# Performance work log

Measured on AMD Instinct MI355X. Metric: run time of the kernel, lower is better.

The kernel has to match this reference:

```python
import jax, jax.numpy as jnp
import numpy as np

EPS = 1e-12  # match torch BCE's protection against log(0)


def setup_inputs() -> dict:
    key = jax.random.key(0)
    k1, k2 = jax.random.split(key)
    n = 8192
    # Pstar is the BCE `input` (prediction) -> must be in (0,1)
    Pstar = jax.random.uniform(k1, (n, n), dtype=jnp.float32)
    pred_pos = jax.random.uniform(k2, (n, 3), dtype=jnp.float32)
    return {"Pstar": Pstar, "pred_pos": pred_pos}


def compute_low_dim_adj(y):
    # Student-t / Cauchy affinity kernel: Q_ij = 1 / (1 + ||y_i - y_j||^2)
    sq = jnp.sum(y * y, axis=1)                      # [n]
    d2 = sq[:, None] + sq[None, :] - 2.0 * (y @ y.T)  # [n, n]
    d2 = jnp.maximum(d2, 0.0)
    return 1.0 / (1.0 + d2)


def reference(Pstar, pred_pos):
    Q = compute_low_dim_adj(pred_pos)  # target in (0,1]
    # F.binary_cross_entropy(input=Pstar, target=Q, reduction='mean')
    P = jnp.clip(Pstar, EPS, 1.0 - EPS)
    ce = -jnp.mean(Q * jnp.log(P) + (1.0 - Q) * jnp.log1p(-P))
    return ce, pred_pos
```

## Files before the change

kernel.cpp:

```cpp
#include <hip/hip_runtime.h>

constexpr int NN   = 8192;
constexpr int ROWS = 16;
constexpr int COLS = 1024;
constexpr int NBLK = (NN / ROWS) * (NN / COLS);
constexpr int COPYBLKS = (NN * 3) / 256;


__global__ __launch_bounds__(256, 8)
void bce_tsne_kernel(const float* __restrict__ Pstar,
                     const float* __restrict__ pos,
                     float* __restrict__ out)
{
    __shared__ float4 rowC[ROWS];
    __shared__ float  waveSum[4];

    const int tid = threadIdx.x;
    const int bid = blockIdx.x;
    const int rowBase = (bid >> 3) * ROWS;
    const int colBase = (bid & 7) * COLS;

    if (tid < ROWS) {
        const int i = rowBase + tid;
        const float y0 = pos[i * 3 + 0];
        const float y1 = pos[i * 3 + 1];
        const float y2 = pos[i * 3 + 2];
        rowC[tid] = make_float4(fmaf(y0, y0, fmaf(y1, y1, y2 * y2)),
                                -2.0f * y0, -2.0f * y1, -2.0f * y2);
    }

    const int j0 = colBase + tid * 4;
    const float4 f0 = *(const float4*)(pos + (size_t)j0 * 3);
    const float4 f1 = *(const float4*)(pos + (size_t)j0 * 3 + 4);
    const float4 f2 = *(const float4*)(pos + (size_t)j0 * 3 + 8);
    float ya[4] = {f0.x, f0.w, f1.z, f2.y};
    float yb[4] = {f0.y, f1.x, f1.w, f2.z};
    float yc[4] = {f0.z, f1.y, f2.x, f2.w};
    float sq[4];
    #pragma unroll
    for (int e = 0; e < 4; ++e)
        sq[e] = fmaf(ya[e], ya[e], fmaf(yb[e], yb[e], yc[e] * yc[e]));

    __syncthreads();

    float acc[4] = {0.0f, 0.0f, 0.0f, 0.0f};
    const float* prow = Pstar + (size_t)rowBase * NN + j0;

    #pragma unroll 4
    for (int r = 0; r < ROWS; ++r) {
        const float4 c  = rowC[r];
        const float4 p4 = *(const float4*)(prow + (size_t)r * NN);
        const float pp[4] = {p4.x, p4.y, p4.z, p4.w};
        #pragma unroll
        for (int e = 0; e < 4; ++e) {
            float d2 = c.x + sq[e];
            d2 = fmaf(c.y, ya[e], d2);
            d2 = fmaf(c.z, yb[e], d2);
            d2 = fmaf(c.w, yc[e], d2);
            d2 = fmaxf(d2, 0.0f);
            const float q  = __builtin_amdgcn_rcpf(1.0f + d2);
            const float p  = fmaxf(pp[e], 1e-12f);
            const float lp = __log2f(p);
            const float lm = __log2f(1.0f - p);
            acc[e] = fmaf(q, lp - lm, acc[e] + lm);
        }
    }

    float a = (acc[0] + acc[1]) + (acc[2] + acc[3]);
    #pragma unroll
    for (int off = 32; off > 0; off >>= 1)
        a += __shfl_down(a, off);
    const int lane = tid & 63;
    const int wid  = tid >> 6;
    if (lane == 0) waveSum[wid] = a;
    __syncthreads();
    if (tid == 0) {
        const float bp = waveSum[0] + waveSum[1] + waveSum[2] + waveSum[3];
        atomicAdd(out, bp * (-0.69314718055994531f / 67108864.0f));
    }

    if (bid < COPYBLKS) {
        const int k = bid * 256 + tid;
        out[1 + k] = pos[k];
    }
}

extern "C" void kernel_launch(void* const* d_in, const int* in_sizes, int n_in,
                              void* d_out, int out_size, void* d_ws, size_t ws_size,
                              hipStream_t stream) {
    const float* Pstar = (const float*)d_in[0];
    const float* pos   = (const float*)d_in[1];
    float* out = (float*)d_out;

    hipMemsetAsync(out, 0, sizeof(float), stream);
    bce_tsne_kernel<<<NBLK, 256, 0, stream>>>(Pstar, pos, out);
}
```

Before: 362.3 us.

## Double-buffer Pstar row loads, double rows per block, fold +1 into row constant

Each block now handles 32 rows instead of 16, which halves the grid and the number of atomics. Rows are processed in groups of four, and the next group's float4 loads are issued before the current group is computed, so memory latency is explicitly software-pipelined. The +1 of the Cauchy kernel is folded into the per-row constant, with the clamp changed to max(w, 1), which saves one add per element. Launch bounds are relaxed from 8 to 4 waves per EU to make room for the extra registers the buffers need, so occupancy may drop.

```diff
diff --git a/kernel.cpp b/kernel.cpp
--- a/kernel.cpp
+++ b/kernel.cpp
@@ -1,13 +1,35 @@
 #include <hip/hip_runtime.h>
 
 constexpr int NN   = 8192;
-constexpr int ROWS = 16;
+constexpr int ROWS = 32;
 constexpr int COLS = 1024;
 constexpr int NBLK = (NN / ROWS) * (NN / COLS);
 constexpr int COPYBLKS = (NN * 3) / 256;
+constexpr int GROUPS = ROWS / 4;
 
 
-__global__ __launch_bounds__(256, 8)
+__device__ __forceinline__ void bce4(const float4 p4, const float4 c,
+                                     const float ya[4], const float yb[4],
+                                     const float yc[4], const float sq[4],
+                                     float acc[4])
+{
+    const float pp[4] = {p4.x, p4.y, p4.z, p4.w};
+    #pragma unroll
+    for (int e = 0; e < 4; ++e) {
+        float w = c.x + sq[e];
+        w = fmaf(c.y, ya[e], w);
+        w = fmaf(c.z, yb[e], w);
+        w = fmaf(c.w, yc[e], w);
+        w = fmaxf(w, 1.0f);
+        const float q  = __builtin_amdgcn_rcpf(w);
+        const float p  = fmaxf(pp[e], 1e-12f);
+        const float lp = __log2f(p);
+        const float lm = __log2f(1.0f - p);
+        acc[e] = fmaf(q, lp - lm, acc[e] + lm);
+    }
+}
+
+__global__ __launch_bounds__(256, 4)
 void bce_tsne_kernel(const float* __restrict__ Pstar,
                      const float* __restrict__ pos,
                      float* __restrict__ out)
@@ -25,7 +47,7 @@
         const float y0 = pos[i * 3 + 0];
         const float y1 = pos[i * 3 + 1];
         const float y2 = pos[i * 3 + 2];
-        rowC[tid] = make_float4(fmaf(y0, y0, fmaf(y1, y1, y2 * y2)),
+        rowC[tid] = make_float4(fmaf(y0, y0, fmaf(y1, y1, fmaf(y2, y2, 1.0f))),
                                 -2.0f * y0, -2.0f * y1, -2.0f * y2);
     }
 
@@ -46,25 +68,26 @@
     float acc[4] = {0.0f, 0.0f, 0.0f, 0.0f};
     const float* prow = Pstar + (size_t)rowBase * NN + j0;
 
-    #pragma unroll 4
-    for (int r = 0; r < ROWS; ++r) {
-        const float4 c  = rowC[r];
-        const float4 p4 = *(const float4*)(prow + (size_t)r * NN);
-        const float pp[4] = {p4.x, p4.y, p4.z, p4.w};
+    float4 bufA[4];
+    #pragma unroll
+    for (int k = 0; k < 4; ++k)
+        bufA[k] = *(const float4*)(prow + (size_t)k * NN);
+
+    for (int g = 0; g < GROUPS - 1; ++g) {
+        float4 bufB[4];
+        const float* pn = prow + (size_t)(g + 1) * 4 * NN;
         #pragma unroll
-        for (int e = 0; e < 4; ++e) {
-            float d2 = c.x + sq[e];
-            d2 = fmaf(c.y, ya[e], d2);
-            d2 = fmaf(c.z, yb[e], d2);
-            d2 = fmaf(c.w, yc[e], d2);
-            d2 = fmaxf(d2, 0.0f);
-            const float q  = __builtin_amdgcn_rcpf(1.0f + d2);
-            const float p  = fmaxf(pp[e], 1e-12f);
-            const float lp = __log2f(p);
-            const float lm = __log2f(1.0f - p);
-            acc[e] = fmaf(q, lp - lm, acc[e] + lm);
-        }
+        for (int k = 0; k < 4; ++k)
+            bufB[k] = *(const float4*)(pn + (size_t)k * NN);
+        #pragma unroll
+        for (int k = 0; k < 4; ++k)
+            bce4(bufA[k], rowC[g * 4 + k], ya, yb, yc, sq, acc);
+        #pragma unroll
+        for (int k = 0; k < 4; ++k) bufA[k] = bufB[k];
     }
+    #pragma unroll
+    for (int k = 0; k < 4; ++k)
+        bce4(bufA[k], rowC[(GROUPS - 1) * 4 + k], ya, yb, yc, sq, acc);
 
     float a = (acc[0] + acc[1]) + (acc[2] + acc[3]);
     #pragma unroll
```

After: 365.8 us. About the same (+1.0%).
